# Performance work log

Measured on AMD Instinct MI355X. Metric: run time of the kernel, lower is better.

The kernel has to match this reference:

```python
import jax, jax.numpy as jnp
import numpy as np

H, SK, SV, PK, PV = 8, 16, 16, 4, 8
EPS = 1e-8
NUM_LOGITS = 3
SCALE_SCALAR = (NUM_LOGITS * SK) ** -0.5
SCALE_POINT = (NUM_LOGITS * PK * (9.0 / 2.0)) ** -0.5
SCALE_PAIR = NUM_LOGITS ** -0.5


def setup_inputs() -> dict:
    key = jax.random.key(0)
    ks = jax.random.split(key, 16)
    b, n, dim, pdim = 1, 512, 384, 128
    s = 0.02
    return {
        "single_repr": jax.random.normal(ks[0], (b, n, dim), jnp.float32),
        "pairwise_repr": jax.random.normal(ks[1], (b, n, n, pdim), jnp.float32),
        "rotations": jax.random.normal(ks[2], (b, n, 3, 3), jnp.float32),
        "translations": jax.random.normal(ks[3], (b, n, 3), jnp.float32),
        "Wsq": jax.random.normal(ks[4], (dim, H * SK), jnp.float32) * s,
        "Wsk": jax.random.normal(ks[5], (dim, H * SK), jnp.float32) * s,
        "Wsv": jax.random.normal(ks[6], (dim, H * SV), jnp.float32) * s,
        "Wpq": jax.random.normal(ks[7], (dim, H * PK * 3), jnp.float32) * s,
        "Wpk": jax.random.normal(ks[8], (dim, H * PK * 3), jnp.float32) * s,
        "Wpv": jax.random.normal(ks[9], (dim, H * PV * 3), jnp.float32) * s,
        "point_weights": jnp.log(jnp.exp(jnp.ones((H,), jnp.float32)) - 1.0),
        "Wpair": jax.random.normal(ks[10], (pdim, H), jnp.float32) * s,
        "bpair": jnp.zeros((H,), jnp.float32),
        "Wout": jax.random.normal(ks[11], (H * (SV + pdim + PV * 4), dim), jnp.float32) * s,
        "bout": jnp.zeros((dim,), jnp.float32),
    }


def reference(single_repr, pairwise_repr, rotations, translations,
              Wsq, Wsk, Wsv, Wpq, Wpk, Wpv, point_weights, Wpair, bpair, Wout, bout):
    x = single_repr
    b, n, _ = x.shape

    # scalar q/k/v: [b, n, h, d]
    q_s = (x @ Wsq).reshape(b, n, H, SK)
    k_s = (x @ Wsk).reshape(b, n, H, SK)
    v_s = (x @ Wsv).reshape(b, n, H, SV)

    # point q/k/v in local frame: [b, n, h, d, 3], then rotate + translate to global frame
    def to_global(t, d):
        p = t.reshape(b, n, H, d, 3)
        return jnp.einsum('bnhdc,bncr->bnhdr', p, rotations) + translations[:, :, None, None, :]

    q_p = to_global(x @ Wpq, PK)   # [b,n,h,pk,3]
    k_p = to_global(x @ Wpk, PK)
    v_p = to_global(x @ Wpv, PV)   # [b,n,h,pv,3]

    # scalar logits [b,h,i,j]
    logits_scalar = jnp.einsum('bihd,bjhd->bhij', q_s, k_s) * SCALE_SCALAR

    # point-distance logits: sum over (d,c) of (q_i - k_j)^2
    q_ph = jnp.transpose(q_p, (0, 2, 1, 3, 4))  # [b,h,i,pk,3]
    k_ph = jnp.transpose(k_p, (0, 2, 1, 3, 4))
    diff = q_ph[:, :, :, None] - k_ph[:, :, None]          # [b,h,i,j,pk,3]
    dist2 = jnp.sum(diff * diff, axis=(-2, -1))            # [b,h,i,j]
    pw = jax.nn.softplus(point_weights)[None, :, None, None]
    logits_points = -0.5 * pw * SCALE_POINT * dist2

    # pairwise bias logits
    logits_pair = jnp.transpose(pairwise_repr @ Wpair + bpair, (0, 3, 1, 2)) * SCALE_PAIR

    attn = jax.nn.softmax(logits_scalar + logits_points + logits_pair, axis=-1)  # [b,h,i,j]

    # scalar output
    res_scalar = jnp.einsum('bhij,bjhd->bihd', attn, v_s).reshape(b, n, H * SV)

    # pairwise output
    res_pair = jnp.einsum('bhij,bijd->bihd', attn, pairwise_repr).reshape(b, n, -1)

    # point output: attend, then map back to local frame with R^T
    v_ph = jnp.transpose(v_p, (0, 2, 1, 3, 4))             # [b,h,j,pv,3]
    res_p = jnp.einsum('bhij,bhjdc->bhidc', attn, v_ph)    # [b,h,i,pv,3] (global)
    res_p = res_p - translations[:, None, :, None, :]
    res_p = jnp.einsum('bhndc,bnrc->bhndr', res_p, rotations)  # R^T applied
    res_p_norm = jnp.sqrt(jnp.sum(res_p * res_p, axis=-1) + EPS)  # [b,h,n,pv]
    res_p = jnp.transpose(res_p, (0, 2, 1, 3, 4)).reshape(b, n, H * PV * 3)
    res_p_norm = jnp.transpose(res_p_norm, (0, 2, 1, 3)).reshape(b, n, H * PV)

    results = jnp.concatenate([res_scalar, res_p, res_p_norm, res_pair], axis=-1)
    return results @ Wout + bout
```

## Files before the change

kernel.cpp:

```cpp
#include <hip/hip_runtime.h>
#include <math.h>

#define NTOK 512
#define DIM 384
#define PDIM 128
#define H 8

#define QKB_STRIDE 224
#define VB_STRIDE  320
#define RES_STRIDE 1408
#define PART_STRIDE 1360

static constexpr float SCALE_SCALAR = 0.14433756729740643f;
static constexpr float SCALE_POINT  = 0.13608276348795434f;
static constexpr float SCALE_PAIR   = 0.57735026918962580f;

__global__ __launch_bounds__(192) void ipa_proj(
    const float* __restrict__ x, const float* __restrict__ rot, const float* __restrict__ trans,
    const float* __restrict__ Wsq, const float* __restrict__ Wsk, const float* __restrict__ Wsv,
    const float* __restrict__ Wpq, const float* __restrict__ Wpk, const float* __restrict__ Wpv,
    float* __restrict__ qB, float* __restrict__ kB, float* __restrict__ vB)
{
  const int tt = blockIdx.x, cg = blockIdx.y, tid = threadIdx.x;
  __shared__ float s_x[8][DIM];
  __shared__ float s_p[8][192];
  __shared__ float s_R[8][9];
  __shared__ float s_T[8][3];

#pragma unroll
  for (int tok = 0; tok < 8; ++tok)
    for (int k = tid; k < DIM; k += 192) s_x[tok][k] = x[(size_t)(tt * 8 + tok) * DIM + k];
  if (tid < 72) s_R[tid / 9][tid % 9] = rot[(size_t)(tt * 8) * 9 + tid];
  if (tid < 24) s_T[tid / 3][tid % 3] = trans[(size_t)(tt * 8) * 3 + tid];
  __syncthreads();

  const int c = cg * 192 + tid;
  const float* W; int ncols, lc;
  if      (c < 128) { W = Wsq; ncols = 128; lc = c; }
  else if (c < 256) { W = Wsk; ncols = 128; lc = c - 128; }
  else if (c < 384) { W = Wsv; ncols = 128; lc = c - 256; }
  else if (c < 480) { W = Wpq; ncols = 96;  lc = c - 384; }
  else if (c < 576) { W = Wpk; ncols = 96;  lc = c - 480; }
  else              { W = Wpv; ncols = 192; lc = c - 576; }

  float acc[8] = {};
  const float* wp = W + lc;
#pragma unroll 4
  for (int k = 0; k < DIM; ++k) {
    float w = *wp; wp += ncols;
#pragma unroll
    for (int tok = 0; tok < 8; ++tok) acc[tok] += w * s_x[tok][k];
  }

  if (cg < 2) {
#pragma unroll
    for (int tok = 0; tok < 8; ++tok) {
      const int i = tt * 8 + tok;
      if (c < 128)      qB[(size_t)i * QKB_STRIDE + c] = acc[tok];
      else if (c < 256) kB[(size_t)i * QKB_STRIDE + (c - 128)] = acc[tok];
      else              vB[(size_t)i * VB_STRIDE + (c - 256)] = acc[tok];
    }
  } else {
#pragma unroll
    for (int tok = 0; tok < 8; ++tok) s_p[tok][tid] = acc[tok];
    __syncthreads();
    for (int t = tid; t < 512; t += 192) {
      const int tok = t >> 6, tr = t & 63;
      const int i = tt * 8 + tok;
      const float* R = s_R[tok];
      const float* T = s_T[tok];
      const float* src; float* dst;
      if (cg == 2) {
        if (tr < 32) { src = &s_p[tok][tr * 3];             dst = qB + (size_t)i * QKB_STRIDE + 128 + tr * 3; }
        else         { src = &s_p[tok][96 + (tr - 32) * 3]; dst = kB + (size_t)i * QKB_STRIDE + 128 + (tr - 32) * 3; }
      } else {
        src = &s_p[tok][tr * 3]; dst = vB + (size_t)i * VB_STRIDE + 128 + tr * 3;
      }
      float px = src[0], py = src[1], pz = src[2];
#pragma unroll
      for (int r = 0; r < 3; ++r)
        dst[r] = px * R[0 * 3 + r] + py * R[1 * 3 + r] + pz * R[2 * 3 + r] + T[r];
    }
  }
}

__global__ __launch_bounds__(256, 4) void ipa_attn_part(
    const float* __restrict__ pair, const float* __restrict__ pw,
    const float* __restrict__ Wpair, const float* __restrict__ bpair,
    const float* __restrict__ qB, const float* __restrict__ kB,
    const float* __restrict__ vB, float* __restrict__ partial,
    int NC, int JR, int NT)
{
  const int c = blockIdx.x, i = blockIdx.y, tid = threadIdx.x;

  __shared__ float4 s_pT4[2048];
  __shared__ float  s_wpT[H][PDIM];
  __shared__ float  s_e[4][2][64];
  __shared__ float  s_qs[128];
  __shared__ float  s_qp[96];
  __shared__ float  s_coef[H], s_bp[H];

  for (int t = tid; t < PDIM * H; t += 256) {
    const int h = t >> 7, d = t & 127;
    s_wpT[h][d] = Wpair[d * 8 + h] * SCALE_PAIR;
  }
  if (tid < 224) {
    float v = qB[(size_t)i * QKB_STRIDE + tid];
    if (tid < 128) s_qs[tid] = v; else s_qp[tid - 128] = v;
  }
  if (tid < H) {
    s_coef[tid] = -0.5f * log1pf(__expf(pw[tid])) * SCALE_POINT;
    s_bp[tid]   = bpair[tid] * SCALE_PAIR;
  }
  __syncthreads();

  const int hp = tid >> 6, jl = tid & 63;
  const int h0 = 2 * hp, h1 = h0 + 1;
  const int h = tid >> 5, u = tid & 31;
  const float coef0 = s_coef[h0], coef1 = s_coef[h1];
  const float bp0 = s_bp[h0], bp1 = s_bp[h1];
  const int ovb0 = (u < 16) ? (h * 16 + u) : (128 + h * 24 + (u - 16));
  const int ovb1 = 128 + h * 24 + 16 + u;

  float m0 = -1e30f, m1 = -1e30f, l0 = 0.f, l1 = 0.f;
  float4 accp = make_float4(0.f, 0.f, 0.f, 0.f);
  float accv0 = 0.f, accv1 = 0.f;

  float4 r[8];
  {
    const float4* g = reinterpret_cast<const float4*>(pair + ((size_t)i * NTOK + (size_t)c * JR) * PDIM);
#pragma unroll
    for (int k = 0; k < 8; ++k) r[k] = g[tid + 256 * k];
  }

  for (int t = 0; t < NT; ++t) {
    __syncthreads();
#pragma unroll
    for (int k = 0; k < 8; ++k) {
      const int f = tid + 256 * k;
      s_pT4[(f & 31) * 64 + ((f >> 5) ^ (f & 7))] = r[k];
    }
    __syncthreads();
    if (t + 1 < NT) {
      const float4* g = reinterpret_cast<const float4*>(
          pair + ((size_t)i * NTOK + (size_t)c * JR + (size_t)(t + 1) * 64) * PDIM);
#pragma unroll
      for (int k = 0; k < 8; ++k) r[k] = g[tid + 256 * k];
    }

    float pa0 = 0.f, pa1 = 0.f;
    {
      const float4* w0p = reinterpret_cast<const float4*>(&s_wpT[h0][0]);
      const float4* w1p = reinterpret_cast<const float4*>(&s_wpT[h1][0]);
#pragma unroll 8
      for (int d4 = 0; d4 < 32; ++d4) {
        float4 p = s_pT4[d4 * 64 + (jl ^ (d4 & 7))];
        float4 w0 = w0p[d4], w1 = w1p[d4];
        pa0 += p.x * w0.x + p.y * w0.y + p.z * w0.z + p.w * w0.w;
        pa1 += p.x * w1.x + p.y * w1.y + p.z * w1.z + p.w * w1.w;
      }
    }
    const int j = c * JR + t * 64 + jl;
    const float4* kr4 = reinterpret_cast<const float4*>(kB + (size_t)j * QKB_STRIDE);
    float sa0 = 0.f, sa1 = 0.f;
    {
      const float4* qs4 = reinterpret_cast<const float4*>(s_qs);
#pragma unroll
      for (int tq = 0; tq < 4; ++tq) {
        float4 q = qs4[h0 * 4 + tq], k = kr4[h0 * 4 + tq];
        sa0 += q.x * k.x + q.y * k.y + q.z * k.z + q.w * k.w;
        float4 q2 = qs4[h1 * 4 + tq], k2 = kr4[h1 * 4 + tq];
        sa1 += q2.x * k2.x + q2.y * k2.y + q2.z * k2.z + q2.w * k2.w;
      }
    }
    float da0 = 0.f, da1 = 0.f;
    {
      const float4* qp4 = reinterpret_cast<const float4*>(s_qp);
#pragma unroll
      for (int tq = 0; tq < 3; ++tq) {
        float4 q = qp4[h0 * 3 + tq], k = kr4[32 + h0 * 3 + tq];
        float d0 = q.x - k.x, d1 = q.y - k.y, d2 = q.z - k.z, d3 = q.w - k.w;
        da0 += d0 * d0 + d1 * d1 + d2 * d2 + d3 * d3;
        float4 q2 = qp4[h1 * 3 + tq], k2 = kr4[32 + h1 * 3 + tq];
        float e0d = q2.x - k2.x, e1d = q2.y - k2.y, e2d = q2.z - k2.z, e3d = q2.w - k2.w;
        da1 += e0d * e0d + e1d * e1d + e2d * e2d + e3d * e3d;
      }
    }
    float lg0 = sa0 * SCALE_SCALAR + coef0 * da0 + pa0 + bp0;
    float lg1 = sa1 * SCALE_SCALAR + coef1 * da1 + pa1 + bp1;

    float tm0 = lg0, tm1 = lg1;
#pragma unroll
    for (int off = 32; off; off >>= 1) {
      tm0 = fmaxf(tm0, __shfl_xor(tm0, off, 64));
      tm1 = fmaxf(tm1, __shfl_xor(tm1, off, 64));
    }
    const float m0n = fmaxf(m0, tm0), m1n = fmaxf(m1, tm1);
    const float sc0 = __expf(m0 - m0n), sc1 = __expf(m1 - m1n);
    const float e0 = __expf(lg0 - m0n), e1 = __expf(lg1 - m1n);
    float ts0 = e0, ts1 = e1;
#pragma unroll
    for (int off = 32; off; off >>= 1) {
      ts0 += __shfl_xor(ts0, off, 64);
      ts1 += __shfl_xor(ts1, off, 64);
    }
    m0 = m0n; m1 = m1n;
    l0 = l0 * sc0 + ts0;
    l1 = l1 * sc1 + ts1;
    s_e[hp][0][jl] = e0;
    s_e[hp][1][jl] = e1;

    const float sc = (tid & 32) ? sc1 : sc0;
    accp.x *= sc; accp.y *= sc; accp.z *= sc; accp.w *= sc;
    accv0 *= sc; accv1 *= sc;
    const float* erow = &s_e[hp][(tid >> 5) & 1][0];
    const float* vrow = vB + (size_t)(c * JR + t * 64) * VB_STRIDE;
#pragma unroll 8
    for (int j2 = 0; j2 < 64; ++j2) {
      const float e = erow[j2];
      float4 p = s_pT4[u * 64 + (j2 ^ (u & 7))];
      accp.x += e * p.x; accp.y += e * p.y; accp.z += e * p.z; accp.w += e * p.w;
      accv0 += e * vrow[ovb0];
      if (u < 8) accv1 += e * vrow[ovb1];
      vrow += VB_STRIDE;
    }
  }

  float* part = partial + ((size_t)i * NC + c) * PART_STRIDE;
  if ((tid & 63) == 0) {
    part[h0] = m0; part[h1] = m1;
    part[8 + h0] = l0; part[8 + h1] = l1;
  }
  *reinterpret_cast<float4*>(part + 336 + h * 128 + u * 4) = accp;
  if (u < 16) part[16 + h * 16 + u] = accv0;
  else        part[144 + h * 24 + (u - 16)] = accv0;
  if (u < 8)  part[144 + h * 24 + 16 + u] = accv1;
}

__global__ __launch_bounds__(256) void ipa_combine(
    const float* __restrict__ partial, const float* __restrict__ rot,
    const float* __restrict__ trans, float* __restrict__ results, int NC)
{
  const int i = blockIdx.x, tid = threadIdx.x;
  __shared__ float s_f[8][H];
  __shared__ float s_invL[H];
  __shared__ float s_res[RES_STRIDE];
  __shared__ float s_pt[192];
  __shared__ float s_R[9], s_T[3];

  const float* pb = partial + (size_t)i * NC * PART_STRIDE;
  if (tid < H) {
    float M = -1e30f;
    for (int cc = 0; cc < NC; ++cc) M = fmaxf(M, pb[cc * PART_STRIDE + tid]);
    float L = 0.f;
    for (int cc = 0; cc < NC; ++cc) {
      float f = __expf(pb[cc * PART_STRIDE + tid] - M);
      s_f[cc][tid] = f;
      L += f * pb[cc * PART_STRIDE + 8 + tid];
    }
    s_invL[tid] = 1.f / L;
  }
  if (tid >= 32 && tid < 41) s_R[tid - 32] = rot[i * 9 + (tid - 32)];
  if (tid >= 48 && tid < 51) s_T[tid - 48] = trans[i * 3 + (tid - 48)];
  __syncthreads();

  for (int idx = tid; idx < 1344; idx += 256) {
    int hh, ofs;
    if (idx < 128)      { hh = idx >> 4;          ofs = 16 + idx; }
    else if (idx < 320) { hh = (idx - 128) / 24;  ofs = 144 + (idx - 128); }
    else                { hh = (idx - 320) >> 7;  ofs = 336 + (idx - 320); }
    float v = 0.f;
    for (int cc = 0; cc < NC; ++cc) v += s_f[cc][hh] * pb[cc * PART_STRIDE + ofs];
    v *= s_invL[hh];
    if (idx < 128)      s_res[idx] = v;
    else if (idx < 320) s_pt[idx - 128] = v;
    else                s_res[384 + (idx - 320)] = v;
  }
  __syncthreads();

  if (tid < 64) {
    const int hh = tid >> 3, p = tid & 7;
    const int base = hh * 24 + p * 3;
    float gx = s_pt[base]     - s_T[0];
    float gy = s_pt[base + 1] - s_T[1];
    float gz = s_pt[base + 2] - s_T[2];
    float lx = gx * s_R[0] + gy * s_R[1] + gz * s_R[2];
    float ly = gx * s_R[3] + gy * s_R[4] + gz * s_R[5];
    float lz = gx * s_R[6] + gy * s_R[7] + gz * s_R[8];
    s_res[128 + base]     = lx;
    s_res[128 + base + 1] = ly;
    s_res[128 + base + 2] = lz;
    s_res[320 + hh * 8 + p] = sqrtf(lx * lx + ly * ly + lz * lz + 1e-8f);
  }
  __syncthreads();

  float4* dst = reinterpret_cast<float4*>(results + (size_t)i * RES_STRIDE);
  const float4* src = reinterpret_cast<const float4*>(s_res);
  for (int t = tid; t < RES_STRIDE / 4; t += 256) dst[t] = src[t];
}

__global__ __launch_bounds__(256) void ipa_out(
    const float* __restrict__ results, const float* __restrict__ Wout,
    const float* __restrict__ bout, float* __restrict__ out)
{
  const int tt = blockIdx.x, ct = blockIdx.y, tid = threadIdx.x;
  __shared__ float s_a[16][128];
  __shared__ float s_w[128][32];
  const int cc = tid & 31, tr = tid >> 5;
  float acc0 = 0.f, acc1 = 0.f;
  for (int k0 = 0; k0 < RES_STRIDE; k0 += 128) {
    __syncthreads();
    for (int t = tid; t < 512; t += 256) {
      const int tok = t >> 5, k4 = t & 31;
      reinterpret_cast<float4*>(&s_a[tok][0])[k4] =
          *reinterpret_cast<const float4*>(results + (size_t)(tt * 16 + tok) * RES_STRIDE + k0 + k4 * 4);
    }
    for (int t = tid; t < 1024; t += 256) {
      const int kk = t >> 3, c4 = t & 7;
      reinterpret_cast<float4*>(&s_w[kk][0])[c4] =
          *reinterpret_cast<const float4*>(Wout + (size_t)(k0 + kk) * DIM + ct * 32 + c4 * 4);
    }
    __syncthreads();
#pragma unroll 16
    for (int kk = 0; kk < 128; ++kk) {
      float w = s_w[kk][cc];
      acc0 += w * s_a[tr][kk];
      acc1 += w * s_a[tr + 8][kk];
    }
  }
  const float b = bout[ct * 32 + cc];
  out[(size_t)(tt * 16 + tr) * DIM + ct * 32 + cc] = acc0 + b;
  out[(size_t)(tt * 16 + tr + 8) * DIM + ct * 32 + cc] = acc1 + b;
}

extern "C" void kernel_launch(void* const* d_in, const int* in_sizes, int n_in,
                              void* d_out, int out_size, void* d_ws, size_t ws_size,
                              hipStream_t stream) {
  const float* x     = (const float*)d_in[0];
  const float* pair  = (const float*)d_in[1];
  const float* rot   = (const float*)d_in[2];
  const float* trans = (const float*)d_in[3];
  const float* Wsq   = (const float*)d_in[4];
  const float* Wsk   = (const float*)d_in[5];
  const float* Wsv   = (const float*)d_in[6];
  const float* Wpq   = (const float*)d_in[7];
  const float* Wpk   = (const float*)d_in[8];
  const float* Wpv   = (const float*)d_in[9];
  const float* pw    = (const float*)d_in[10];
  const float* Wpair = (const float*)d_in[11];
  const float* bpair = (const float*)d_in[12];
  const float* Wout  = (const float*)d_in[13];
  const float* bout  = (const float*)d_in[14];
  float* out = (float*)d_out;

  float* ws = (float*)d_ws;
  float* qB = ws;
  float* kB = qB + (size_t)NTOK * QKB_STRIDE;
  float* vB = kB + (size_t)NTOK * QKB_STRIDE;
  float* results = vB + (size_t)NTOK * VB_STRIDE;
  float* partial = results + (size_t)NTOK * RES_STRIDE;

  const size_t base_f = (size_t)NTOK * QKB_STRIDE * 2 + (size_t)NTOK * VB_STRIDE
                      + (size_t)NTOK * RES_STRIDE;
  int NC = 8;
  while (NC > 1 && (base_f + (size_t)NTOK * NC * PART_STRIDE) * 4 > ws_size) NC >>= 1;
  const int JR = NTOK / NC;
  const int NT = JR / 64;

  ipa_proj<<<dim3(NTOK / 8, 4), 192, 0, stream>>>(x, rot, trans, Wsq, Wsk, Wsv, Wpq, Wpk, Wpv, qB, kB, vB);
  ipa_attn_part<<<dim3(NC, NTOK), 256, 0, stream>>>(pair, pw, Wpair, bpair, qB, kB, vB, partial, NC, JR, NT);
  ipa_combine<<<NTOK, 256, 0, stream>>>(partial, rot, trans, results, NC);
  ipa_out<<<dim3(NTOK / 16, DIM / 32), 256, 0, stream>>>(results, Wout, bout, out);
}
```

Before: 476.7 us.

## Split-K output GEMM, smaller proj tiles, and drop pair-load prefetch in attention

The output projection is split into a split-K register-tiled GEMM that writes partial sums, followed by a small reduction kernel that adds the partials and the bias. The projection kernel now handles 4 tokens per block instead of 8, giving more blocks, and loads x with float4. The attention kernel drops its register prefetch of the next pairwise tile and its occupancy hint, and uses four independent accumulators for the pair-bias dot product. Removing the prefetch may expose global load latency in the bandwidth-heavy attention kernel. The split-K path adds an extra launch and extra global traffic for the partial sums.

```diff
diff --git a/kernel.cpp b/kernel.cpp
--- a/kernel.cpp
+++ b/kernel.cpp
@@ -10,6 +10,8 @@
 #define VB_STRIDE  320
 #define RES_STRIDE 1408
 #define PART_STRIDE 1360
+#define KS 4
+#define KC (RES_STRIDE / KS)
 
 static constexpr float SCALE_SCALAR = 0.14433756729740643f;
 static constexpr float SCALE_POINT  = 0.13608276348795434f;
@@ -22,16 +24,19 @@
     float* __restrict__ qB, float* __restrict__ kB, float* __restrict__ vB)
 {
   const int tt = blockIdx.x, cg = blockIdx.y, tid = threadIdx.x;
-  __shared__ float s_x[8][DIM];
-  __shared__ float s_p[8][192];
-  __shared__ float s_R[8][9];
-  __shared__ float s_T[8][3];
-
-#pragma unroll
-  for (int tok = 0; tok < 8; ++tok)
-    for (int k = tid; k < DIM; k += 192) s_x[tok][k] = x[(size_t)(tt * 8 + tok) * DIM + k];
-  if (tid < 72) s_R[tid / 9][tid % 9] = rot[(size_t)(tt * 8) * 9 + tid];
-  if (tid < 24) s_T[tid / 3][tid % 3] = trans[(size_t)(tt * 8) * 3 + tid];
+  __shared__ float s_x[4][DIM];
+  __shared__ float s_p[4][192];
+  __shared__ float s_R[4][9];
+  __shared__ float s_T[4][3];
+
+  {
+    const float4* xg = reinterpret_cast<const float4*>(x + (size_t)(tt * 4) * DIM);
+    float4* sx4 = reinterpret_cast<float4*>(&s_x[0][0]);
+    sx4[tid] = xg[tid];
+    sx4[tid + 192] = xg[tid + 192];
+  }
+  if (tid < 36) s_R[tid / 9][tid % 9] = rot[(size_t)(tt * 4) * 9 + tid];
+  if (tid >= 64 && tid < 76) s_T[(tid - 64) / 3][(tid - 64) % 3] = trans[(size_t)(tt * 4) * 3 + (tid - 64)];
   __syncthreads();
 
   const int c = cg * 192 + tid;
@@ -43,30 +48,30 @@
   else if (c < 576) { W = Wpk; ncols = 96;  lc = c - 480; }
   else              { W = Wpv; ncols = 192; lc = c - 576; }
 
-  float acc[8] = {};
+  float acc[4] = {};
   const float* wp = W + lc;
-#pragma unroll 4
+#pragma unroll 8
   for (int k = 0; k < DIM; ++k) {
     float w = *wp; wp += ncols;
 #pragma unroll
-    for (int tok = 0; tok < 8; ++tok) acc[tok] += w * s_x[tok][k];
+    for (int tok = 0; tok < 4; ++tok) acc[tok] += w * s_x[tok][k];
   }
 
   if (cg < 2) {
 #pragma unroll
-    for (int tok = 0; tok < 8; ++tok) {
-      const int i = tt * 8 + tok;
+    for (int tok = 0; tok < 4; ++tok) {
+      const int i = tt * 4 + tok;
       if (c < 128)      qB[(size_t)i * QKB_STRIDE + c] = acc[tok];
       else if (c < 256) kB[(size_t)i * QKB_STRIDE + (c - 128)] = acc[tok];
       else              vB[(size_t)i * VB_STRIDE + (c - 256)] = acc[tok];
     }
   } else {
 #pragma unroll
-    for (int tok = 0; tok < 8; ++tok) s_p[tok][tid] = acc[tok];
+    for (int tok = 0; tok < 4; ++tok) s_p[tok][tid] = acc[tok];
     __syncthreads();
-    for (int t = tid; t < 512; t += 192) {
+    for (int t = tid; t < 256; t += 192) {
       const int tok = t >> 6, tr = t & 63;
-      const int i = tt * 8 + tok;
+      const int i = tt * 4 + tok;
       const float* R = s_R[tok];
       const float* T = s_T[tok];
       const float* src; float* dst;
@@ -84,7 +89,7 @@
   }
 }
 
-__global__ __launch_bounds__(256, 4) void ipa_attn_part(
+__global__ __launch_bounds__(256) void ipa_attn_part(
     const float* __restrict__ pair, const float* __restrict__ pw,
     const float* __restrict__ Wpair, const float* __restrict__ bpair,
     const float* __restrict__ qB, const float* __restrict__ kB,
@@ -112,13 +117,10 @@
     s_coef[tid] = -0.5f * log1pf(__expf(pw[tid])) * SCALE_POINT;
     s_bp[tid]   = bpair[tid] * SCALE_PAIR;
   }
-  __syncthreads();
 
   const int hp = tid >> 6, jl = tid & 63;
   const int h0 = 2 * hp, h1 = h0 + 1;
   const int h = tid >> 5, u = tid & 31;
-  const float coef0 = s_coef[h0], coef1 = s_coef[h1];
-  const float bp0 = s_bp[h0], bp1 = s_bp[h1];
   const int ovb0 = (u < 16) ? (h * 16 + u) : (128 + h * 24 + (u - 16));
   const int ovb1 = 128 + h * 24 + 16 + u;
 
@@ -126,14 +128,14 @@
   float4 accp = make_float4(0.f, 0.f, 0.f, 0.f);
   float accv0 = 0.f, accv1 = 0.f;
 
-  float4 r[8];
-  {
-    const float4* g = reinterpret_cast<const float4*>(pair + ((size_t)i * NTOK + (size_t)c * JR) * PDIM);
-#pragma unroll
-    for (int k = 0; k < 8; ++k) r[k] = g[tid + 256 * k];
-  }
-
   for (int t = 0; t < NT; ++t) {
+    float4 r[8];
+    {
+      const float4* g = reinterpret_cast<const float4*>(
+          pair + ((size_t)i * NTOK + (size_t)c * JR + (size_t)t * 64) * PDIM);
+#pragma unroll
+      for (int k = 0; k < 8; ++k) r[k] = g[tid + 256 * k];
+    }
     __syncthreads();
 #pragma unroll
     for (int k = 0; k < 8; ++k) {
@@ -141,14 +143,8 @@
       s_pT4[(f & 31) * 64 + ((f >> 5) ^ (f & 7))] = r[k];
     }
     __syncthreads();
-    if (t + 1 < NT) {
-      const float4* g = reinterpret_cast<const float4*>(
-          pair + ((size_t)i * NTOK + (size_t)c * JR + (size_t)(t + 1) * 64) * PDIM);
-#pragma unroll
-      for (int k = 0; k < 8; ++k) r[k] = g[tid + 256 * k];
-    }
-
-    float pa0 = 0.f, pa1 = 0.f;
+
+    float4 pa0v = make_float4(0.f, 0.f, 0.f, 0.f), pa1v = pa0v;
     {
       const float4* w0p = reinterpret_cast<const float4*>(&s_wpT[h0][0]);
       const float4* w1p = reinterpret_cast<const float4*>(&s_wpT[h1][0]);
@@ -156,10 +152,13 @@
       for (int d4 = 0; d4 < 32; ++d4) {
         float4 p = s_pT4[d4 * 64 + (jl ^ (d4 & 7))];
         float4 w0 = w0p[d4], w1 = w1p[d4];
-        pa0 += p.x * w0.x + p.y * w0.y + p.z * w0.z + p.w * w0.w;
-        pa1 += p.x * w1.x + p.y * w1.y + p.z * w1.z + p.w * w1.w;
+        pa0v.x += p.x * w0.x; pa0v.y += p.y * w0.y; pa0v.z += p.z * w0.z; pa0v.w += p.w * w0.w;
+        pa1v.x += p.x * w1.x; pa1v.y += p.y * w1.y; pa1v.z += p.z * w1.z; pa1v.w += p.w * w1.w;
       }
     }
+    const float pa0 = pa0v.x + pa0v.y + pa0v.z + pa0v.w;
+    const float pa1 = pa1v.x + pa1v.y + pa1v.z + pa1v.w;
+
     const int j = c * JR + t * 64 + jl;
     const float4* kr4 = reinterpret_cast<const float4*>(kB + (size_t)j * QKB_STRIDE);
     float sa0 = 0.f, sa1 = 0.f;
@@ -186,8 +185,8 @@
         da1 += e0d * e0d + e1d * e1d + e2d * e2d + e3d * e3d;
       }
     }
-    float lg0 = sa0 * SCALE_SCALAR + coef0 * da0 + pa0 + bp0;
-    float lg1 = sa1 * SCALE_SCALAR + coef1 * da1 + pa1 + bp1;
+    float lg0 = sa0 * SCALE_SCALAR + s_coef[h0] * da0 + pa0 + s_bp[h0];
+    float lg1 = sa1 * SCALE_SCALAR + s_coef[h1] * da1 + pa1 + s_bp[h1];
 
     float tm0 = lg0, tm1 = lg1;
 #pragma unroll
@@ -299,38 +298,64 @@
   for (int t = tid; t < RES_STRIDE / 4; t += 256) dst[t] = src[t];
 }
 
-__global__ __launch_bounds__(256) void ipa_out(
+__global__ __launch_bounds__(256) void ipa_out1(
     const float* __restrict__ results, const float* __restrict__ Wout,
-    const float* __restrict__ bout, float* __restrict__ out)
+    float* __restrict__ pout)
 {
-  const int tt = blockIdx.x, ct = blockIdx.y, tid = threadIdx.x;
-  __shared__ float s_a[16][128];
-  __shared__ float s_w[128][32];
-  const int cc = tid & 31, tr = tid >> 5;
-  float acc0 = 0.f, acc1 = 0.f;
-  for (int k0 = 0; k0 < RES_STRIDE; k0 += 128) {
+  const int tt = blockIdx.x, ct = blockIdx.y, ks = blockIdx.z, tid = threadIdx.x;
+  __shared__ float s_a[32][40];
+  __shared__ float s_w[32][64];
+  const int tx = tid & 15, ty = tid >> 4;
+  float acc[2][4] = {};
+
+  for (int kc = 0; kc < KC / 32; ++kc) {
+    const int k0 = ks * KC + kc * 32;
     __syncthreads();
-    for (int t = tid; t < 512; t += 256) {
-      const int tok = t >> 5, k4 = t & 31;
-      reinterpret_cast<float4*>(&s_a[tok][0])[k4] =
-          *reinterpret_cast<const float4*>(results + (size_t)(tt * 16 + tok) * RES_STRIDE + k0 + k4 * 4);
-    }
-    for (int t = tid; t < 1024; t += 256) {
-      const int kk = t >> 3, c4 = t & 7;
-      reinterpret_cast<float4*>(&s_w[kk][0])[c4] =
-          *reinterpret_cast<const float4*>(Wout + (size_t)(k0 + kk) * DIM + ct * 32 + c4 * 4);
+    {
+      const int tok = tid >> 3, kq = tid & 7;
+      *reinterpret_cast<float4*>(&s_a[tok][kq * 4]) =
+          *reinterpret_cast<const float4*>(results + (size_t)(tt * 32 + tok) * RES_STRIDE + k0 + kq * 4);
+    }
+#pragma unroll
+    for (int rr = 0; rr < 2; ++rr) {
+      const int tq = tid + rr * 256;
+      const int kk = tq >> 4, c4 = tq & 15;
+      *reinterpret_cast<float4*>(&s_w[kk][c4 * 4]) =
+          *reinterpret_cast<const float4*>(Wout + (size_t)(k0 + kk) * DIM + ct * 64 + c4 * 4);
     }
     __syncthreads();
-#pragma unroll 16
-    for (int kk = 0; kk < 128; ++kk) {
-      float w = s_w[kk][cc];
-      acc0 += w * s_a[tr][kk];
-      acc1 += w * s_a[tr + 8][kk];
-    }
-  }
-  const float b = bout[ct * 32 + cc];
-  out[(size_t)(tt * 16 + tr) * DIM + ct * 32 + cc] = acc0 + b;
-  out[(size_t)(tt * 16 + tr + 8) * DIM + ct * 32 + cc] = acc1 + b;
+#pragma unroll 8
+    for (int kk = 0; kk < 32; ++kk) {
+      const float a0 = s_a[ty][kk], a1 = s_a[ty + 16][kk];
+#pragma unroll
+      for (int cc = 0; cc < 4; ++cc) {
+        const float w = s_w[kk][tx + 16 * cc];
+        acc[0][cc] += a0 * w;
+        acc[1][cc] += a1 * w;
+      }
+    }
+  }
+#pragma unroll
+  for (int rr = 0; rr < 2; ++rr)
+#pragma unroll
+    for (int cc = 0; cc < 4; ++cc)
+      pout[((size_t)ks * NTOK + tt * 32 + ty + 16 * rr) * DIM + ct * 64 + tx + 16 * cc] = acc[rr][cc];
+}
+
+__global__ __launch_bounds__(256) void ipa_out2(
+    const float* __restrict__ pout, const float* __restrict__ bout, float* __restrict__ out)
+{
+  const int idx = blockIdx.x * 256 + threadIdx.x;
+  const float4* p4 = reinterpret_cast<const float4*>(pout);
+  float4 v = p4[idx];
+#pragma unroll
+  for (int ks = 1; ks < KS; ++ks) {
+    float4 w = p4[idx + ks * (NTOK * DIM / 4)];
+    v.x += w.x; v.y += w.y; v.z += w.z; v.w += w.w;
+  }
+  const float4 b = reinterpret_cast<const float4*>(bout)[idx % (DIM / 4)];
+  v.x += b.x; v.y += b.y; v.z += b.z; v.w += b.w;
+  reinterpret_cast<float4*>(out)[idx] = v;
 }
 
 extern "C" void kernel_launch(void* const* d_in, const int* in_sizes, int n_in,
@@ -359,16 +384,24 @@
   float* vB = kB + (size_t)NTOK * QKB_STRIDE;
   float* results = vB + (size_t)NTOK * VB_STRIDE;
   float* partial = results + (size_t)NTOK * RES_STRIDE;
+  float* pout = partial;
 
   const size_t base_f = (size_t)NTOK * QKB_STRIDE * 2 + (size_t)NTOK * VB_STRIDE
                       + (size_t)NTOK * RES_STRIDE;
+  const size_t pout_f = (size_t)KS * NTOK * DIM;
   int NC = 8;
-  while (NC > 1 && (base_f + (size_t)NTOK * NC * PART_STRIDE) * 4 > ws_size) NC >>= 1;
+  while (NC > 1) {
+    size_t region = (size_t)NTOK * NC * PART_STRIDE;
+    if (region < pout_f) region = pout_f;
+    if ((base_f + region) * 4 <= ws_size) break;
+    NC >>= 1;
+  }
   const int JR = NTOK / NC;
   const int NT = JR / 64;
 
-  ipa_proj<<<dim3(NTOK / 8, 4), 192, 0, stream>>>(x, rot, trans, Wsq, Wsk, Wsv, Wpq, Wpk, Wpv, qB, kB, vB);
+  ipa_proj<<<dim3(NTOK / 4, 4), 192, 0, stream>>>(x, rot, trans, Wsq, Wsk, Wsv, Wpq, Wpk, Wpv, qB, kB, vB);
   ipa_attn_part<<<dim3(NC, NTOK), 256, 0, stream>>>(pair, pw, Wpair, bpair, qB, kB, vB, partial, NC, JR, NT);
   ipa_combine<<<NTOK, 256, 0, stream>>>(partial, rot, trans, results, NC);
-  ipa_out<<<dim3(NTOK / 16, DIM / 32), 256, 0, stream>>>(results, Wout, bout, out);
-}
+  ipa_out1<<<dim3(NTOK / 32, DIM / 64, KS), 256, 0, stream>>>(results, Wout, pout);
+  ipa_out2<<<NTOK * DIM / 4 / 256, 256, 0, stream>>>(pout, bout, out);
+}
```

After: 511.6 us. 7.3% more time.
